# Kernel tuning notes

Measured on AMD Instinct MI355X. Metric: run time of the kernel, lower is better.

Reference implementation:

```python
import jax, jax.numpy as jnp
import numpy as np

NUM_HEADS = 16


def setup_inputs() -> dict:
    key = jax.random.key(0)
    ks = jax.random.split(key, 5)
    B, S, D = 4, 2048, 1024
    scale = 1.0 / np.sqrt(D)
    return {
        "x": jax.random.normal(ks[0], (B, S, D), dtype=jnp.float32),
        "q_proj": jax.random.normal(ks[1], (D, D), dtype=jnp.float32) * scale,
        "k_proj": jax.random.normal(ks[2], (D, D), dtype=jnp.float32) * scale,
        "v_proj": jax.random.normal(ks[3], (D, D), dtype=jnp.float32) * scale,
        "o_proj": jax.random.normal(ks[4], (D, D), dtype=jnp.float32) * scale,
    }


def reference(x, q_proj, k_proj, v_proj, o_proj):
    B, S, D = x.shape
    H = NUM_HEADS
    hd = D // H
    # projections: weight is [d_out, d_in]
    q = jnp.einsum('bsd,kd->bsk', x, q_proj)
    k = jnp.einsum('bsd,kd->bsk', x, k_proj)
    v = jnp.einsum('bsd,kd->bsk', x, v_proj)
    # split heads: [B, H, S, hd]
    q = q.reshape(B, S, H, hd).transpose(0, 2, 1, 3)
    k = k.reshape(B, S, H, hd).transpose(0, 2, 1, 3)
    v = v.reshape(B, S, H, hd).transpose(0, 2, 1, 3)
    scores = jnp.einsum('bhqd,bhkd->bhqk', q, k) / jnp.sqrt(jnp.asarray(hd, dtype=x.dtype))
    causal = jnp.tril(jnp.ones((S, S), dtype=bool))  # True = keep
    scores = jnp.where(causal, scores, -jnp.inf)
    attn = jax.nn.softmax(scores, axis=-1)
    out = jnp.einsum('bhqk,bhkd->bhqd', attn, v)
    out = out.transpose(0, 2, 1, 3).reshape(B, S, D)
    return jnp.einsum('bsv,mv->bsm', out, o_proj)
```

## Files before the change

### kernel.cpp

```cpp
#include <hip/hip_runtime.h>
#include <hip/hip_bf16.h>
#include <stdint.h>


typedef __bf16 bf16x8 __attribute__((ext_vector_type(8)));
typedef __bf16 bf16x4 __attribute__((ext_vector_type(4)));
typedef float  f32x4  __attribute__((ext_vector_type(4)));

static __device__ __forceinline__ f32x4 mfma16(bf16x8 a, bf16x8 b, f32x4 c) {
  return __builtin_amdgcn_mfma_f32_16x16x32_bf16(a, b, c, 0, 0, 0);
}

static __device__ __forceinline__ void load16_lds(const void* g, void* l) {
  __builtin_amdgcn_global_load_lds(
      (const __attribute__((address_space(1))) unsigned int*)g,
      (__attribute__((address_space(3))) unsigned int*)l, 16, 0, 0);
}

__global__ __launch_bounds__(256) void cvt_f32_bf16(
    const float* __restrict__ in, __bf16* __restrict__ out, int n8) {
  int i = blockIdx.x * blockDim.x + threadIdx.x;
  if (i >= n8) return;
  const float4* in4 = (const float4*)in;
  float4 a = in4[2 * i], b = in4[2 * i + 1];
  __bf16 v[8];
  v[0] = (__bf16)a.x; v[1] = (__bf16)a.y; v[2] = (__bf16)a.z; v[3] = (__bf16)a.w;
  v[4] = (__bf16)b.x; v[5] = (__bf16)b.y; v[6] = (__bf16)b.z; v[7] = (__bf16)b.w;
  *(bf16x8*)(out + 8 * i) = *(bf16x8*)v;
}

__global__ __launch_bounds__(256) void cvt_w(
    const float* __restrict__ w0, const float* __restrict__ w1,
    const float* __restrict__ w2, const float* __restrict__ w3,
    __bf16* __restrict__ wqkv, __bf16* __restrict__ wo) {
  int blk = blockIdx.x;
  int m = blk >> 9;
  const float* src = (m == 0) ? w0 : (m == 1) ? w1 : (m == 2) ? w2 : w3;
  __bf16* dst = (m < 3) ? (wqkv + (size_t)m * (1024 * 1024)) : wo;
  const float scl = (m == 0) ? 0.18033688011112042f : 1.0f;
  int i = (blk & 511) * 256 + threadIdx.x;
  const float4* in4 = (const float4*)src;
  float4 a = in4[2 * i], b = in4[2 * i + 1];
  __bf16 v[8];
  v[0] = (__bf16)(a.x * scl); v[1] = (__bf16)(a.y * scl);
  v[2] = (__bf16)(a.z * scl); v[3] = (__bf16)(a.w * scl);
  v[4] = (__bf16)(b.x * scl); v[5] = (__bf16)(b.y * scl);
  v[6] = (__bf16)(b.z * scl); v[7] = (__bf16)(b.w * scl);
  *(bf16x8*)(dst + 8 * i) = *(bf16x8*)v;
}

static __device__ __forceinline__ void stage_unit(
    const __bf16* __restrict__ X, long grow0, int K, long k0,
    __bf16* lds, int t) {
  const int lane = t & 63, w = t >> 6;
  const int rl = w * 8 + (lane >> 3);
  const int chunk = (lane & 7) ^ ((lane >> 3) & 7);
  load16_lds(X + (grow0 + rl) * (long)K + k0 + chunk * 8,
             lds + (w * 8) * 64);
}

template <typename OutT>
__global__ __launch_bounds__(512, 2) void gemm_bt8(
    const __bf16* __restrict__ A, const __bf16* __restrict__ Bw,
    OutT* __restrict__ C, int M, int N, int K, int NX) {
  __shared__ __align__(16) __bf16 As[3][256 * 64];
  __shared__ __align__(16) __bf16 Bs[3][128 * 64];
  const int t = threadIdx.x;
  const int lane = t & 63, w = t >> 6;
  const int wm = w >> 1, wn = w & 1;
  const int l15 = lane & 15, quad = lane >> 4;

  const int bid = blockIdx.x;
  const int cpx = gridDim.x >> 3;
  const int swz = (bid & 7) * cpx + (bid >> 3);
  const long m0 = (long)(swz / NX) * 256;
  const long n0 = (long)(swz % NX) * 128;

  int aoff[4][2], boff[4][2];
#pragma unroll
  for (int mf = 0; mf < 4; mf++)
#pragma unroll
    for (int ks = 0; ks < 2; ks++)
      aoff[mf][ks] = (wm * 64 + mf * 16 + l15) * 64 + (((ks * 4 + quad) ^ (l15 & 7)) << 3);
#pragma unroll
  for (int nf = 0; nf < 4; nf++)
#pragma unroll
    for (int ks = 0; ks < 2; ks++)
      boff[nf][ks] = (wn * 64 + nf * 16 + l15) * 64 + (((ks * 4 + quad) ^ (l15 & 7)) << 3);

  const int NT = K >> 6;
  __bf16 *Ac = As[0], *An = As[1], *Asg = As[2];
  __bf16 *Bc = Bs[0], *Bn = Bs[1], *Bsg = Bs[2];

#pragma unroll
  for (int u = 0; u < 4; u++) stage_unit(A, m0 + u * 64, K, 0, Ac + u * 64 * 64, t);
#pragma unroll
  for (int u = 0; u < 2; u++) stage_unit(Bw, n0 + u * 64, K, 0, Bc + u * 64 * 64, t);
#pragma unroll
  for (int u = 0; u < 4; u++) stage_unit(A, m0 + u * 64, K, 64, An + u * 64 * 64, t);
#pragma unroll
  for (int u = 0; u < 2; u++) stage_unit(Bw, n0 + u * 64, K, 64, Bn + u * 64 * 64, t);
  asm volatile("s_waitcnt vmcnt(6)" ::: "memory");
  __builtin_amdgcn_s_barrier();

  f32x4 acc[4][4] = {};
  for (int T = 0; T < NT; T++) {
    const bool pf2 = (T + 2 < NT);
    const long kn2 = (long)(T + 2) * 64;

    bf16x8 bfr[4][2];
#pragma unroll
    for (int nf = 0; nf < 4; nf++)
#pragma unroll
      for (int ks = 0; ks < 2; ks++)
        bfr[nf][ks] = *(const bf16x8*)(Bc + boff[nf][ks]);
    {
      bf16x8 a00 = *(const bf16x8*)(Ac + aoff[0][0]);
      bf16x8 a01 = *(const bf16x8*)(Ac + aoff[0][1]);
      bf16x8 a10 = *(const bf16x8*)(Ac + aoff[1][0]);
      bf16x8 a11 = *(const bf16x8*)(Ac + aoff[1][1]);
      if (pf2) {
#pragma unroll
        for (int u = 0; u < 4; u++)
          stage_unit(A, m0 + u * 64, K, kn2, Asg + u * 64 * 64, t);
      }
      __builtin_amdgcn_s_barrier();
      asm volatile("s_waitcnt lgkmcnt(0)" ::: "memory");
      __builtin_amdgcn_sched_barrier(0);
      __builtin_amdgcn_s_setprio(1);
#pragma unroll
      for (int nf = 0; nf < 4; nf++) {
        acc[0][nf] = mfma16(a00, bfr[nf][0], acc[0][nf]);
        acc[0][nf] = mfma16(a01, bfr[nf][1], acc[0][nf]);
        acc[1][nf] = mfma16(a10, bfr[nf][0], acc[1][nf]);
        acc[1][nf] = mfma16(a11, bfr[nf][1], acc[1][nf]);
      }
      __builtin_amdgcn_s_setprio(0);
      __builtin_amdgcn_s_barrier();
    }
    {
      bf16x8 a00 = *(const bf16x8*)(Ac + aoff[2][0]);
      bf16x8 a01 = *(const bf16x8*)(Ac + aoff[2][1]);
      bf16x8 a10 = *(const bf16x8*)(Ac + aoff[3][0]);
      bf16x8 a11 = *(const bf16x8*)(Ac + aoff[3][1]);
      if (pf2) {
#pragma unroll
        for (int u = 0; u < 2; u++)
          stage_unit(Bw, n0 + u * 64, K, kn2, Bsg + u * 64 * 64, t);
        asm volatile("s_waitcnt vmcnt(6)" ::: "memory");
      } else {
        asm volatile("s_waitcnt vmcnt(0)" ::: "memory");
      }
      __builtin_amdgcn_s_barrier();
      asm volatile("s_waitcnt lgkmcnt(0)" ::: "memory");
      __builtin_amdgcn_sched_barrier(0);
      __builtin_amdgcn_s_setprio(1);
#pragma unroll
      for (int nf = 0; nf < 4; nf++) {
        acc[2][nf] = mfma16(a00, bfr[nf][0], acc[2][nf]);
        acc[2][nf] = mfma16(a01, bfr[nf][1], acc[2][nf]);
        acc[3][nf] = mfma16(a10, bfr[nf][0], acc[3][nf]);
        acc[3][nf] = mfma16(a11, bfr[nf][1], acc[3][nf]);
      }
      __builtin_amdgcn_s_setprio(0);
      __builtin_amdgcn_s_barrier();
    }
    __bf16* ta = Ac; Ac = An; An = Asg; Asg = ta;
    __bf16* tb = Bc; Bc = Bn; Bn = Bsg; Bsg = tb;
  }

#pragma unroll
  for (int mf = 0; mf < 4; mf++)
#pragma unroll
    for (int nf = 0; nf < 4; nf++)
#pragma unroll
      for (int r = 0; r < 4; r++) {
        long row = m0 + wm * 64 + mf * 16 + quad * 4 + r;
        long col = n0 + wn * 64 + nf * 16 + l15;
        float v = acc[mf][nf][r];
        if constexpr (sizeof(OutT) == 2) C[row * (long)N + col] = (OutT)(__bf16)v;
        else                             C[row * (long)N + col] = v;
      }
}

__global__ __launch_bounds__(256) void vtrans(
    const __bf16* __restrict__ QKV, __bf16* __restrict__ VT) {
  constexpr int LDs = 136;
  __shared__ __align__(16) __bf16 Ts[64 * LDs];
  const int t = threadIdx.x;
  const int st0 = blockIdx.x * 128, h = blockIdx.y, b = blockIdx.z;
  const long vbase = (long)b * 2048 * 3072 + 2048 + h * 64;
#pragma unroll
  for (int i = 0; i < 4; i++) {
    int sl = i * 32 + (t >> 3), d0 = (t & 7) * 8;
    __bf16 tmp[8];
    *(uint4*)tmp = *(const uint4*)(QKV + vbase + (long)(st0 + sl) * 3072 + d0);
#pragma unroll
    for (int j = 0; j < 8; j++) Ts[(d0 + j) * LDs + sl] = tmp[j];
  }
  __syncthreads();
  const long obase = (long)(b * 16 + h) * 64 * 2048 + st0;
  const int d = t >> 2;
#pragma unroll
  for (int i = 0; i < 4; i++) {
    int sc = ((t & 3) + 4 * i) * 8;
    *(uint4*)(VT + obase + (long)d * 2048 + sc) = *(const uint4*)(Ts + d * LDs + sc);
  }
}

__global__ __launch_bounds__(256) void attn4(
    const __bf16* __restrict__ QKV, const __bf16* __restrict__ VT,
    __bf16* __restrict__ O) {
  constexpr int SD = 3072;
  constexpr int LDP = 72;
  __shared__ __align__(16) __bf16 Ks[2][64 * 64];
  __shared__ __align__(16) __bf16 Vs[2][64 * 64];
  __shared__ __align__(16) __bf16 Pw[4 * 32 * LDP];
  const int t = threadIdx.x;
  const int lane = t & 63, w = t >> 6;
  const int l15 = lane & 15, quad = lane >> 4;
  const int jj = blockIdx.x, h = blockIdx.y, b = blockIdx.z;
  const long qbase = (long)b * 2048 * SD + h * 64;
  const long kbase = qbase + 1024;
  const long vtbase = (long)(b * 16 + h) * 64 * 2048;
  __bf16* Pme = Pw + w * 32 * LDP;

  const int sr = w * 16 + (lane >> 3);
  const int scg = (lane & 7) ^ (sr & 7);
  const int ldsOff = (w * 16) * 64;
  const __bf16* gK = QKV + kbase + (long)sr * SD + scg * 8;
  const __bf16* gV = VT + vtbase + (long)sr * 2048 + scg * 8;

  int kvoff[4][2];
#pragma unroll
  for (int nt = 0; nt < 4; nt++)
#pragma unroll
    for (int kk = 0; kk < 2; kk++)
      kvoff[nt][kk] = (nt * 16 + l15) * 64 + (((kk * 4 + quad) ^ (l15 & 7)) << 3);

  bf16x8 ones;
#pragma unroll
  for (int j = 0; j < 8; j++) ones[j] = (__bf16)1.0f;

#pragma unroll
  for (int half = 0; half < 2; half++) {
    const int qt = half ? (15 - jj) : jj;
    const int q0 = qt * 128;
    const int wrow0 = q0 + w * 32;

    bf16x8 qf[2][2];
#pragma unroll
    for (int mt = 0; mt < 2; mt++)
#pragma unroll
      for (int kk = 0; kk < 2; kk++)
        qf[mt][kk] = *(const bf16x8*)(QKV + qbase +
            (long)(wrow0 + mt * 16 + l15) * SD + kk * 32 + quad * 8);

    f32x4 o_acc[2][4] = {};
    f32x4 o_l[2] = {};

    const int nkt = 2 * qt + 2;

    __syncthreads();
    load16_lds(gK, Ks[0] + ldsOff);
    load16_lds(gK + 8 * SD, Ks[0] + ldsOff + 8 * 64);
    load16_lds(gV, Vs[0] + ldsOff);
    load16_lds(gV + 8 * 2048, Vs[0] + ldsOff + 8 * 64);

    int cur = 0;
    for (int kt = 0; kt < nkt; kt++) {
      __syncthreads();
      if (kt + 1 < nkt) {
        const __bf16* gKn = gK + (long)(kt + 1) * 64 * SD;
        const __bf16* gVn = gV + (kt + 1) * 64;
        __bf16* lk = Ks[cur ^ 1] + ldsOff;
        __bf16* lv = Vs[cur ^ 1] + ldsOff;
        load16_lds(gKn, lk);
        load16_lds(gKn + 8 * SD, lk + 8 * 64);
        load16_lds(gVn, lv);
        load16_lds(gVn + 8 * 2048, lv + 8 * 64);
      }

      const int k0 = kt * 64;
      if (k0 <= wrow0 + 31) {
        const __bf16* KsB = Ks[cur];
        const __bf16* VsB = Vs[cur];
        bf16x8 kf[4][2];
#pragma unroll
        for (int nt = 0; nt < 4; nt++)
#pragma unroll
          for (int kk = 0; kk < 2; kk++)
            kf[nt][kk] = *(const bf16x8*)(KsB + kvoff[nt][kk]);
        f32x4 st[4][2];
        __builtin_amdgcn_s_setprio(1);
#pragma unroll
        for (int nt = 0; nt < 4; nt++)
#pragma unroll
          for (int mt = 0; mt < 2; mt++) {
            f32x4 z = {0.f, 0.f, 0.f, 0.f};
            z = mfma16(kf[nt][0], qf[mt][0], z);
            st[nt][mt] = mfma16(kf[nt][1], qf[mt][1], z);
          }
        __builtin_amdgcn_s_setprio(0);

        if (k0 + 63 <= wrow0) {
#pragma unroll
          for (int mt = 0; mt < 2; mt++)
#pragma unroll
            for (int nt = 0; nt < 4; nt++) {
              bf16x4 pb;
#pragma unroll
              for (int r = 0; r < 4; r++)
                pb[r] = (__bf16)__builtin_amdgcn_exp2f(st[nt][mt][r]);
              *(bf16x4*)(Pme + (mt * 16 + l15) * LDP + nt * 16 + quad * 4) = pb;
            }
        } else {
#pragma unroll
          for (int mt = 0; mt < 2; mt++) {
            const int qrow = wrow0 + mt * 16 + l15;
#pragma unroll
            for (int nt = 0; nt < 4; nt++) {
              const int keyb = k0 + nt * 16 + quad * 4;
              bf16x4 pb;
#pragma unroll
              for (int r = 0; r < 4; r++) {
                float e = __builtin_amdgcn_exp2f(st[nt][mt][r]);
                if (keyb + r > qrow) e = 0.f;
                pb[r] = (__bf16)e;
              }
              *(bf16x4*)(Pme + (mt * 16 + l15) * LDP + nt * 16 + quad * 4) = pb;
            }
          }
        }

#pragma unroll
        for (int kk = 0; kk < 2; kk++) {
          bf16x8 vf[4];
#pragma unroll
          for (int dt = 0; dt < 4; dt++)
            vf[dt] = *(const bf16x8*)(VsB + kvoff[dt][kk]);
#pragma unroll
          for (int mt = 0; mt < 2; mt++) {
            bf16x8 pf = *(const bf16x8*)(Pme + (mt * 16 + l15) * LDP + kk * 32 + quad * 8);
            __builtin_amdgcn_s_setprio(1);
#pragma unroll
            for (int dt = 0; dt < 4; dt++)
              o_acc[mt][dt] = mfma16(pf, vf[dt], o_acc[mt][dt]);
            o_l[mt] = mfma16(pf, ones, o_l[mt]);
            __builtin_amdgcn_s_setprio(0);
          }
        }
      }
      cur ^= 1;
    }

#pragma unroll
    for (int mt = 0; mt < 2; mt++) {
#pragma unroll
      for (int r = 0; r < 4; r++) {
        float inv = 1.f / o_l[mt][r];
        int row = wrow0 + mt * 16 + quad * 4 + r;
        long ob = ((long)b * 2048 + row) * 1024 + h * 64;
#pragma unroll
        for (int dt = 0; dt < 4; dt++)
          O[ob + dt * 16 + l15] = (__bf16)(o_acc[mt][dt][r] * inv);
      }
    }
  }
}

extern "C" void kernel_launch(void* const* d_in, const int* in_sizes, int n_in,
                              void* d_out, int out_size, void* d_ws, size_t ws_size,
                              hipStream_t stream) {
  const float* x  = (const float*)d_in[0];
  const float* wq = (const float*)d_in[1];
  const float* wk = (const float*)d_in[2];
  const float* wv = (const float*)d_in[3];
  const float* wo = (const float*)d_in[4];
  float* out = (float*)d_out;

  char* ws = (char*)d_ws;
  __bf16* xb   = (__bf16*)(ws);
  __bf16* wqkv = (__bf16*)(ws + (16l << 20));
  __bf16* wob  = (__bf16*)(ws + (22l << 20));
  __bf16* QKV  = (__bf16*)(ws + (24l << 20));
  __bf16* VT   = (__bf16*)(ws + (72l << 20));
  __bf16* Ab   = xb;

  cvt_f32_bf16<<<4096, 256, 0, stream>>>(x, xb, 8192 * 1024 / 8);
  cvt_w<<<2048, 256, 0, stream>>>(wq, wk, wv, wo, wqkv, wob);

  gemm_bt8<__bf16><<<768, 512, 0, stream>>>(xb, wqkv, QKV, 8192, 3072, 1024, 24);

  vtrans<<<dim3(16, 16, 4), 256, 0, stream>>>(QKV, VT);

  attn4<<<dim3(8, 16, 4), 256, 0, stream>>>(QKV, VT, Ab);

  gemm_bt8<float><<<256, 512, 0, stream>>>(Ab, wob, out, 8192, 1024, 1024, 8);
}
```

Before: 248.7 us.

## Triple-buffer K/V tiles in attention with vmcnt waits and remap blocks

Moves the attention kernel's K/V staging from double to triple buffering. It prefetches two tiles ahead and waits with an explicit s_waitcnt vmcnt before a raw barrier, replacing the full __syncthreads. The grid becomes 1D with a remapped block index, which changes how (batch, head, q-block) work is spread across CUs and may improve L2 locality. The cost is more LDS per block, which may lower occupancy, and correctness now depends on the hand-counted vmcnt value.

```diff
diff --git a/kernel.cpp b/kernel.cpp
--- a/kernel.cpp
+++ b/kernel.cpp
@@ -213,13 +213,18 @@
     __bf16* __restrict__ O) {
   constexpr int SD = 3072;
   constexpr int LDP = 72;
-  __shared__ __align__(16) __bf16 Ks[2][64 * 64];
-  __shared__ __align__(16) __bf16 Vs[2][64 * 64];
+  __shared__ __align__(16) __bf16 Ks[3][64 * 64];
+  __shared__ __align__(16) __bf16 Vs[3][64 * 64];
   __shared__ __align__(16) __bf16 Pw[4 * 32 * LDP];
   const int t = threadIdx.x;
   const int lane = t & 63, w = t >> 6;
   const int l15 = lane & 15, quad = lane >> 4;
-  const int jj = blockIdx.x, h = blockIdx.y, b = blockIdx.z;
+
+  const int bid = blockIdx.x;
+  const int g = (bid & 7) * 8 + (bid >> 6);
+  const int jj = (bid >> 3) & 7;
+  const int h = g & 15, b = g >> 4;
+
   const long qbase = (long)b * 2048 * SD + h * 64;
   const long kbase = qbase + 1024;
   const long vtbase = (long)(b * 16 + h) * 64 * 2048;
@@ -266,19 +271,30 @@
     load16_lds(gK + 8 * SD, Ks[0] + ldsOff + 8 * 64);
     load16_lds(gV, Vs[0] + ldsOff);
     load16_lds(gV + 8 * 2048, Vs[0] + ldsOff + 8 * 64);
+    {
+      const __bf16* gK1 = gK + (long)64 * SD;
+      const __bf16* gV1 = gV + 64;
+      load16_lds(gK1, Ks[1] + ldsOff);
+      load16_lds(gK1 + 8 * SD, Ks[1] + ldsOff + 8 * 64);
+      load16_lds(gV1, Vs[1] + ldsOff);
+      load16_lds(gV1 + 8 * 2048, Vs[1] + ldsOff + 8 * 64);
+    }
 
     int cur = 0;
     for (int kt = 0; kt < nkt; kt++) {
-      __syncthreads();
-      if (kt + 1 < nkt) {
-        const __bf16* gKn = gK + (long)(kt + 1) * 64 * SD;
-        const __bf16* gVn = gV + (kt + 1) * 64;
-        __bf16* lk = Ks[cur ^ 1] + ldsOff;
-        __bf16* lv = Vs[cur ^ 1] + ldsOff;
-        load16_lds(gKn, lk);
-        load16_lds(gKn + 8 * SD, lk + 8 * 64);
-        load16_lds(gVn, lv);
-        load16_lds(gVn + 8 * 2048, lv + 8 * 64);
+      if (kt + 1 < nkt) asm volatile("s_waitcnt vmcnt(4)" ::: "memory");
+      else              asm volatile("s_waitcnt vmcnt(0)" ::: "memory");
+      __builtin_amdgcn_s_barrier();
+      __builtin_amdgcn_sched_barrier(0);
+
+      if (kt + 2 < nkt) {
+        int stg = cur + 2; if (stg >= 3) stg -= 3;
+        const __bf16* gKn = gK + (long)(kt + 2) * 64 * SD;
+        const __bf16* gVn = gV + (kt + 2) * 64;
+        load16_lds(gKn, Ks[stg] + ldsOff);
+        load16_lds(gKn + 8 * SD, Ks[stg] + ldsOff + 8 * 64);
+        load16_lds(gVn, Vs[stg] + ldsOff);
+        load16_lds(gVn + 8 * 2048, Vs[stg] + ldsOff + 8 * 64);
       }
 
       const int k0 = kt * 64;
@@ -351,7 +367,7 @@
           }
         }
       }
-      cur ^= 1;
+      cur = (cur == 2) ? 0 : cur + 1;
     }
 
 #pragma unroll
@@ -394,7 +410,7 @@
 
   vtrans<<<dim3(16, 16, 4), 256, 0, stream>>>(QKV, VT);
 
-  attn4<<<dim3(8, 16, 4), 256, 0, stream>>>(QKV, VT, Ab);
+  attn4<<<512, 256, 0, stream>>>(QKV, VT, Ab);
 
   gemm_bt8<float><<<256, 512, 0, stream>>>(Ab, wob, out, 8192, 1024, 1024, 8);
 }
```

Result: faster. 241.8 us (-2.8%).
